# Kernel optimization log

Measured on AMD Instinct MI355X. Metric: run time of the kernel, lower is better.

Reference implementation:

```python
import jax, jax.numpy as jnp
import numpy as np

HIDDEN = 2048
NUM_HEADS = 16
HEAD_DIM = 128
ROPE_THETA = 10000.0


def setup_inputs() -> dict:
    key = jax.random.key(0)
    ks = jax.random.split(key, 5)
    s = 1.0 / np.sqrt(HIDDEN)
    return {
        "hidden_states": jax.random.normal(ks[0], (2, 2048, HIDDEN), dtype=jnp.float32),
        "wq": jax.random.normal(ks[1], (HIDDEN, HIDDEN), dtype=jnp.float32) * s,
        "wk": jax.random.normal(ks[2], (HIDDEN, HIDDEN), dtype=jnp.float32) * s,
        "wv": jax.random.normal(ks[3], (HIDDEN, HIDDEN), dtype=jnp.float32) * s,
        "wo": jax.random.normal(ks[4], (HIDDEN, HIDDEN), dtype=jnp.float32) * s,
    }


def _rope_tables(seq_len, head_dim, dtype):
    pos = jnp.arange(seq_len, dtype=jnp.float32)
    inv_freq = 1.0 / (ROPE_THETA ** (jnp.arange(0, head_dim, 2, dtype=jnp.float32) / head_dim))
    freqs = pos[:, None] * inv_freq[None, :]          # [S, D/2]
    emb = jnp.concatenate([freqs, freqs], axis=-1)    # [S, D]
    return jnp.cos(emb).astype(dtype), jnp.sin(emb).astype(dtype)


def _rotate_half(x):
    x1, x2 = jnp.split(x, 2, axis=-1)
    return jnp.concatenate([-x2, x1], axis=-1)


def reference(hidden_states, wq, wk, wv, wo):
    B, S, H = hidden_states.shape
    nh, hd = NUM_HEADS, HEAD_DIM
    # Projections (torch Linear: x @ W^T); weights stored as [out, in]
    q = (hidden_states @ wq.T).reshape(B, S, nh, hd).transpose(0, 2, 1, 3)  # [B,nh,S,hd]
    k = (hidden_states @ wk.T).reshape(B, S, nh, hd).transpose(0, 2, 1, 3)
    v = (hidden_states @ wv.T).reshape(B, S, nh, hd).transpose(0, 2, 1, 3)
    # Inline RoPE
    cos, sin = _rope_tables(S, hd, q.dtype)           # [S, hd]
    cos = cos[None, None]                             # [1,1,S,hd]
    sin = sin[None, None]
    q = q * cos + _rotate_half(q) * sin
    k = k * cos + _rotate_half(k) * sin
    # Full attention (no mask path; default pos ids)
    scores = jnp.einsum("bhqd,bhkd->bhqk", q, k) / jnp.sqrt(jnp.asarray(hd, q.dtype))
    attn = jax.nn.softmax(scores.astype(jnp.float32), axis=-1).astype(q.dtype)
    out = jnp.einsum("bhqk,bhkd->bhqd", attn, v)      # [B,nh,S,hd]
    out = out.transpose(0, 2, 1, 3).reshape(B, S, nh * hd)
    return out @ wo.T
```

## Files before the change

### kernel.cpp

```cpp
#include <hip/hip_runtime.h>
#include <hip/hip_bf16.h>
#include <math.h>

#define HIDDEN 2048
#define NH 16
#define HD 128
#define SEQ 2048
#define BATCH 2
#define NROW (BATCH*SEQ)

typedef unsigned short u16;
typedef unsigned int   u32;
typedef __bf16 bf16x8 __attribute__((ext_vector_type(8)));
typedef float  f32x4  __attribute__((ext_vector_type(4)));

__device__ __forceinline__ u16 f2bf(float f){
  u32 u = __float_as_uint(f);
  u32 r = (u + 0x7fffu + ((u >> 16) & 1u)) >> 16;
  return (u16)r;
}
__device__ __forceinline__ float bf2f(u16 h){ return __uint_as_float(((u32)h) << 16); }

typedef const void __attribute__((address_space(1)))* gas1_ptr;
typedef void __attribute__((address_space(3)))*       las3_ptr;
__device__ __forceinline__ void gload16(const void* g, void* l){
  __builtin_amdgcn_global_load_lds((gas1_ptr)g, (las3_ptr)l, 16, 0, 0);
}

__global__ void cast_kernel(const float* __restrict__ src, u16* __restrict__ dst, int n4){
  int i = blockIdx.x * blockDim.x + threadIdx.x;
  if (i >= n4) return;
  float4 v = reinterpret_cast<const float4*>(src)[i];
  ushort4 o;
  o.x = f2bf(v.x); o.y = f2bf(v.y); o.z = f2bf(v.z); o.w = f2bf(v.w);
  reinterpret_cast<ushort4*>(dst)[i] = o;
}

__global__ void rope_table_kernel(float* __restrict__ cosT, float* __restrict__ sinT){
  int i = blockIdx.x * blockDim.x + threadIdx.x;
  if (i >= SEQ * 64) return;
  int s = i >> 6, d = i & 63;
  float invf = expf(-(float)d * 0.14391156830f);
  float ang = (float)s * invf;
  float sv, cv;
  sincosf(ang, &sv, &cv);
  cosT[i] = cv; sinT[i] = sv;
}

__global__ void rope_apply_kernel(u16* __restrict__ Q, u16* __restrict__ K,
                                  const float* __restrict__ cosT, const float* __restrict__ sinT){
  int i = blockIdx.x * blockDim.x + threadIdx.x;
  if (i >= NROW * NH * 64) return;
  int d  = i & 63;
  int rh = i >> 6;
  int s  = (rh / NH) & (SEQ - 1);
  size_t base = (size_t)rh * HD;
  float c  = cosT[(s << 6) + d];
  float sn = sinT[(s << 6) + d];
  float q0 = bf2f(Q[base + d]), q1 = bf2f(Q[base + d + 64]);
  float k0 = bf2f(K[base + d]), k1 = bf2f(K[base + d + 64]);
  Q[base + d]      = f2bf(q0 * c - q1 * sn);
  Q[base + d + 64] = f2bf(q1 * c + q0 * sn);
  K[base + d]      = f2bf(k0 * c - k1 * sn);
  K[base + d + 64] = f2bf(k1 * c + k0 * sn);
}

template<int BF16OUT>
__global__ __launch_bounds__(256) void gemm_bt_kernel(
    const u16* __restrict__ A, const u16* __restrict__ B, void* __restrict__ C,
    int M, int N, int K)
{
  __shared__ __align__(16) u16 As[128 * 32];
  __shared__ __align__(16) u16 Bs[128 * 32];
  const int tid  = threadIdx.x;
  const int wid  = tid >> 6;
  const int lane = tid & 63;
  const int lrow = lane & 15, lk = lane >> 4;
  const int wr = wid >> 1, wc = wid & 1;
  const int row0 = blockIdx.x * 128, col0 = blockIdx.y * 128;

  f32x4 acc[4][4];
  #pragma unroll
  for (int m = 0; m < 4; m++)
    #pragma unroll
    for (int n = 0; n < 4; n++) acc[m][n] = (f32x4){0.f, 0.f, 0.f, 0.f};

  const int arow = tid >> 2;
  const int acol = (tid & 3) * 8;
  const u16* Ag = A + (size_t)(row0 + arow) * K + acol;
  const u16* Bg = B + (size_t)(col0 + arow) * K + acol;
  u16* AsW = As + wid * 512;
  u16* BsW = Bs + wid * 512;

  for (int k0 = 0; k0 < K; k0 += 32){
    gload16(Ag + k0,          AsW);
    gload16(Ag + 64 * K + k0, AsW + 2048);
    gload16(Bg + k0,          BsW);
    gload16(Bg + 64 * K + k0, BsW + 2048);
    __syncthreads();
    bf16x8 af[4], bfv[4];
    #pragma unroll
    for (int m = 0; m < 4; m++) af[m]  = *(const bf16x8*)&As[(wr * 64 + m * 16 + lrow) * 32 + lk * 8];
    #pragma unroll
    for (int n = 0; n < 4; n++) bfv[n] = *(const bf16x8*)&Bs[(wc * 64 + n * 16 + lrow) * 32 + lk * 8];
    #pragma unroll
    for (int m = 0; m < 4; m++)
      #pragma unroll
      for (int n = 0; n < 4; n++)
        acc[m][n] = __builtin_amdgcn_mfma_f32_16x16x32_bf16(af[m], bfv[n], acc[m][n], 0, 0, 0);
    __syncthreads();
  }

  #pragma unroll
  for (int m = 0; m < 4; m++){
    const int r = row0 + wr * 64 + m * 16 + lk * 4;
    #pragma unroll
    for (int n = 0; n < 4; n++){
      const int c = col0 + wc * 64 + n * 16 + lrow;
      #pragma unroll
      for (int j = 0; j < 4; j++){
        float v = acc[m][n][j];
        if constexpr (BF16OUT) ((u16*)C)[(size_t)(r + j) * N + c] = f2bf(v);
        else                   ((float*)C)[(size_t)(r + j) * N + c] = v;
      }
    }
  }
}

__global__ __launch_bounds__(256) void attn_kernel(
    const u16* __restrict__ Q, const u16* __restrict__ K,
    const u16* __restrict__ V, u16* __restrict__ O)
{
  __shared__ __align__(16) u16 Ks[32 * 128];
  __shared__ __align__(16) u16 Vt[128 * 32];
  __shared__ __align__(16) u16 Pl[4][16 * 32];
  const int tid = threadIdx.x, wid = tid >> 6, lane = tid & 63;
  const int lrow = lane & 15, lk = lane >> 4;
  const int b = blockIdx.z, h = blockIdx.y;
  const int q0 = blockIdx.x * 64 + wid * 16;

  bf16x8 qf[4];
  const u16* qrow = Q + ((size_t)((b * SEQ + q0 + lrow) * NH) + h) * HD;
  #pragma unroll
  for (int kc = 0; kc < 4; kc++) qf[kc] = *(const bf16x8*)(qrow + kc * 32 + lk * 8);

  f32x4 accO[8];
  #pragma unroll
  for (int i = 0; i < 8; i++) accO[i] = (f32x4){0.f, 0.f, 0.f, 0.f};
  float mrun[4] = {-1e30f, -1e30f, -1e30f, -1e30f};
  float lrun[4] = {0.f, 0.f, 0.f, 0.f};
  const float SC = 0.08838834764831845f * 1.4426950408889634f;

  const int skey = tid >> 4;
  const int spc  = tid & 15;
  const int vkey = tid & 31;
  const int vdel = (tid >> 5) * 8;
  const u16* Kbase = K + ((size_t)(b * SEQ) * NH + h) * HD;
  const u16* Vbase = V + ((size_t)(b * SEQ) * NH + h) * HD;
  u16* KsW = Ks + wid * 512;

  for (int kv = 0; kv < SEQ; kv += 32){
    __syncthreads();
    #pragma unroll
    for (int r = 0; r < 2; r++){
      int key   = r * 16 + skey;
      int cdata = spc ^ (key & 7);
      gload16(Kbase + (size_t)(kv + key) * (NH * HD) + cdata * 8, KsW + r * 2048);
    }
    #pragma unroll
    for (int r = 0; r < 2; r++){
      int dd0 = r * 64 + vdel;
      const u16* g = Vbase + (size_t)(kv + vkey) * (NH * HD) + dd0;
      uint4 vv = *(const uint4*)g;
      #pragma unroll
      for (int j = 0; j < 8; j++){
        u32 word = (j < 2) ? vv.x : (j < 4) ? vv.y : (j < 6) ? vv.z : vv.w;
        u16 val  = (u16)((j & 1) ? (word >> 16) : (word & 0xffff));
        int dd = dd0 + j;
        int c  = (vkey >> 3) ^ ((dd >> 1) & 3);
        Vt[dd * 32 + c * 8 + (vkey & 7)] = val;
      }
    }
    __syncthreads();

    f32x4 accS[2];
    accS[0] = (f32x4){0.f,0.f,0.f,0.f}; accS[1] = (f32x4){0.f,0.f,0.f,0.f};
    #pragma unroll
    for (int ns = 0; ns < 2; ns++){
      int row = ns * 16 + lrow;
      #pragma unroll
      for (int kc = 0; kc < 4; kc++){
        int pc = (kc * 4 + lk) ^ (row & 7);
        bf16x8 kf = *(const bf16x8*)&Ks[row * 128 + pc * 8];
        accS[ns] = __builtin_amdgcn_mfma_f32_16x16x32_bf16(qf[kc], kf, accS[ns], 0, 0, 0);
      }
    }

    float su[2][4], tmax[4];
    #pragma unroll
    for (int j = 0; j < 4; j++){
      su[0][j] = accS[0][j] * SC;
      su[1][j] = accS[1][j] * SC;
      tmax[j]  = fmaxf(su[0][j], su[1][j]);
    }
    #pragma unroll
    for (int j = 0; j < 4; j++){
      #pragma unroll
      for (int m = 1; m < 16; m <<= 1) tmax[j] = fmaxf(tmax[j], __shfl_xor(tmax[j], m));
    }
    float alpha[4], p[2][4];
    #pragma unroll
    for (int j = 0; j < 4; j++){
      float mnew = fmaxf(mrun[j], tmax[j]);
      alpha[j]   = exp2f(mrun[j] - mnew);
      mrun[j]    = mnew;
      p[0][j] = exp2f(su[0][j] - mnew);
      p[1][j] = exp2f(su[1][j] - mnew);
      float rowsum = p[0][j] + p[1][j];
      #pragma unroll
      for (int m = 1; m < 16; m <<= 1) rowsum += __shfl_xor(rowsum, m);
      lrun[j] = lrun[j] * alpha[j] + rowsum;
    }
    #pragma unroll
    for (int dn = 0; dn < 8; dn++)
      #pragma unroll
      for (int j = 0; j < 4; j++) accO[dn][j] *= alpha[j];

    u16* pb = &Pl[wid][0];
    #pragma unroll
    for (int ns = 0; ns < 2; ns++)
      #pragma unroll
      for (int j = 0; j < 4; j++){
        int prow = lk * 4 + j;
        int pcol = ns * 16 + lrow;
        int c = (pcol >> 3) ^ ((prow >> 1) & 3);
        pb[prow * 32 + c * 8 + (pcol & 7)] = f2bf(p[ns][j]);
      }
    int pc2 = lk ^ ((lrow >> 1) & 3);
    bf16x8 pf = *(const bf16x8*)&pb[lrow * 32 + pc2 * 8];

    #pragma unroll
    for (int dn = 0; dn < 8; dn++){
      int row = dn * 16 + lrow;
      int vc = lk ^ ((row >> 1) & 3);
      bf16x8 vf = *(const bf16x8*)&Vt[row * 32 + vc * 8];
      accO[dn] = __builtin_amdgcn_mfma_f32_16x16x32_bf16(pf, vf, accO[dn], 0, 0, 0);
    }
  }

  #pragma unroll
  for (int dn = 0; dn < 8; dn++){
    #pragma unroll
    for (int j = 0; j < 4; j++){
      int qq = q0 + lk * 4 + j;
      float v = accO[dn][j] / lrun[j];
      O[((size_t)(b * SEQ + qq) * NH + h) * HD + dn * 16 + lrow] = f2bf(v);
    }
  }
}

extern "C" void kernel_launch(void* const* d_in, const int* in_sizes, int n_in,
                              void* d_out, int out_size, void* d_ws, size_t ws_size,
                              hipStream_t stream){
  const float* hs = (const float*)d_in[0];
  const float* wq = (const float*)d_in[1];
  const float* wk = (const float*)d_in[2];
  const float* wv = (const float*)d_in[3];
  const float* wo = (const float*)d_in[4];
  float* out = (float*)d_out;

  char* ws = (char*)d_ws;
  const size_t NEL_HS = (size_t)NROW * HIDDEN;
  const size_t NEL_W  = (size_t)HIDDEN * HIDDEN;
  u16* hsb = (u16*)ws; ws += NEL_HS * 2;
  u16* wqb = (u16*)ws; ws += NEL_W * 2;
  u16* wkb = (u16*)ws; ws += NEL_W * 2;
  u16* wvb = (u16*)ws; ws += NEL_W * 2;
  u16* wob = (u16*)ws; ws += NEL_W * 2;
  u16* qb  = (u16*)ws; ws += NEL_HS * 2;
  u16* kb  = (u16*)ws; ws += NEL_HS * 2;
  u16* vb  = (u16*)ws; ws += NEL_HS * 2;
  u16* ab  = (u16*)ws; ws += NEL_HS * 2;
  float* cosT = (float*)ws; ws += (size_t)SEQ * 64 * 4;
  float* sinT = (float*)ws; ws += (size_t)SEQ * 64 * 4;

  cast_kernel<<<dim3((unsigned)(NEL_HS / 4 / 256)), dim3(256), 0, stream>>>(hs, hsb, (int)(NEL_HS / 4));
  cast_kernel<<<dim3((unsigned)(NEL_W  / 4 / 256)), dim3(256), 0, stream>>>(wq, wqb, (int)(NEL_W / 4));
  cast_kernel<<<dim3((unsigned)(NEL_W  / 4 / 256)), dim3(256), 0, stream>>>(wk, wkb, (int)(NEL_W / 4));
  cast_kernel<<<dim3((unsigned)(NEL_W  / 4 / 256)), dim3(256), 0, stream>>>(wv, wvb, (int)(NEL_W / 4));
  cast_kernel<<<dim3((unsigned)(NEL_W  / 4 / 256)), dim3(256), 0, stream>>>(wo, wob, (int)(NEL_W / 4));
  rope_table_kernel<<<dim3(SEQ * 64 / 256), dim3(256), 0, stream>>>(cosT, sinT);
  gemm_bt_kernel<1><<<dim3(NROW / 128, HIDDEN / 128), dim3(256), 0, stream>>>(hsb, wqb, qb, NROW, HIDDEN, HIDDEN);
  gemm_bt_kernel<1><<<dim3(NROW / 128, HIDDEN / 128), dim3(256), 0, stream>>>(hsb, wkb, kb, NROW, HIDDEN, HIDDEN);
  gemm_bt_kernel<1><<<dim3(NROW / 128, HIDDEN / 128), dim3(256), 0, stream>>>(hsb, wvb, vb, NROW, HIDDEN, HIDDEN);
  rope_apply_kernel<<<dim3(NROW * NH * 64 / 256), dim3(256), 0, stream>>>(qb, kb, cosT, sinT);
  attn_kernel<<<dim3(SEQ / 64, NH, BATCH), dim3(256), 0, stream>>>(qb, kb, vb, ab);
  gemm_bt_kernel<0><<<dim3(NROW / 128, HIDDEN / 128), dim3(256), 0, stream>>>(ab, wob, out, NROW, HIDDEN, HIDDEN);
}
```

Before: 623.6 us.

## Restructure flash attention with transposed score MFMA, 64-key tiles, and ds_read_tr for V

```diff
diff --git a/kernel.cpp b/kernel.cpp
--- a/kernel.cpp
+++ b/kernel.cpp
@@ -11,6 +11,7 @@
 
 typedef unsigned short u16;
 typedef unsigned int   u32;
+typedef unsigned long long u64;
 typedef __bf16 bf16x8 __attribute__((ext_vector_type(8)));
 typedef float  f32x4  __attribute__((ext_vector_type(4)));
 
@@ -131,130 +132,140 @@
     const u16* __restrict__ Q, const u16* __restrict__ K,
     const u16* __restrict__ V, u16* __restrict__ O)
 {
-  __shared__ __align__(16) u16 Ks[32 * 128];
-  __shared__ __align__(16) u16 Vt[128 * 32];
-  __shared__ __align__(16) u16 Pl[4][16 * 32];
+  __shared__ __align__(128) u16 Ks[64 * 128];
+  __shared__ __align__(128) u16 Vs[64 * 128];
   const int tid = threadIdx.x, wid = tid >> 6, lane = tid & 63;
   const int lrow = lane & 15, lk = lane >> 4;
   const int b = blockIdx.z, h = blockIdx.y;
-  const int q0 = blockIdx.x * 64 + wid * 16;
+  const int q0w = blockIdx.x * 64 + wid * 16;
+
+  const float SCL = 0.08838834764831845f * 1.4426950408889634f;
 
   bf16x8 qf[4];
-  const u16* qrow = Q + ((size_t)((b * SEQ + q0 + lrow) * NH) + h) * HD;
-  #pragma unroll
-  for (int kc = 0; kc < 4; kc++) qf[kc] = *(const bf16x8*)(qrow + kc * 32 + lk * 8);
+  {
+    const u16* qrow = Q + ((size_t)((b * SEQ + q0w + lrow) * NH) + h) * HD;
+    #pragma unroll
+    for (int kc = 0; kc < 4; kc++){
+      union { bf16x8 v; u16 s[8]; } u;
+      u.v = *(const bf16x8*)(qrow + kc * 32 + lk * 8);
+      #pragma unroll
+      for (int j = 0; j < 8; j++) u.s[j] = f2bf(bf2f(u.s[j]) * SCL);
+      qf[kc] = u.v;
+    }
+  }
 
   f32x4 accO[8];
   #pragma unroll
   for (int i = 0; i < 8; i++) accO[i] = (f32x4){0.f, 0.f, 0.f, 0.f};
-  float mrun[4] = {-1e30f, -1e30f, -1e30f, -1e30f};
-  float lrun[4] = {0.f, 0.f, 0.f, 0.f};
-  const float SC = 0.08838834764831845f * 1.4426950408889634f;
-
-  const int skey = tid >> 4;
-  const int spc  = tid & 15;
-  const int vkey = tid & 31;
-  const int vdel = (tid >> 5) * 8;
-  const u16* Kbase = K + ((size_t)(b * SEQ) * NH + h) * HD;
-  const u16* Vbase = V + ((size_t)(b * SEQ) * NH + h) * HD;
-  u16* KsW = Ks + wid * 512;
-
-  for (int kv = 0; kv < SEQ; kv += 32){
+  float mrun = -1e30f, lrun = 0.f;
+
+  const u16* Kbase = K + (size_t)(b * SEQ) * (NH * HD) + h * HD;
+  const u16* Vbase = V + (size_t)(b * SEQ) * (NH * HD) + h * HD;
+  const u32 vsbase = (u32)(size_t)(las3_ptr)&Vs[0];
+  const u32 vaddr  = vsbase + (u32)(lk * 1024 + lrow * 8);
+
+  const int ksub = lane >> 4;
+  const int kchk = lane & 15;
+  const int vsub = (lane >> 1) & 3;
+  const int vd   = (lane >> 3) * 16 + (lane & 1) * 8;
+
+  for (int kv = 0; kv < SEQ; kv += 64){
     __syncthreads();
     #pragma unroll
-    for (int r = 0; r < 2; r++){
-      int key   = r * 16 + skey;
-      int cdata = spc ^ (key & 7);
-      gload16(Kbase + (size_t)(kv + key) * (NH * HD) + cdata * 8, KsW + r * 2048);
-    }
-    #pragma unroll
-    for (int r = 0; r < 2; r++){
-      int dd0 = r * 64 + vdel;
-      const u16* g = Vbase + (size_t)(kv + vkey) * (NH * HD) + dd0;
-      uint4 vv = *(const uint4*)g;
-      #pragma unroll
-      for (int j = 0; j < 8; j++){
-        u32 word = (j < 2) ? vv.x : (j < 4) ? vv.y : (j < 6) ? vv.z : vv.w;
-        u16 val  = (u16)((j & 1) ? (word >> 16) : (word & 0xffff));
-        int dd = dd0 + j;
-        int c  = (vkey >> 3) ^ ((dd >> 1) & 3);
-        Vt[dd * 32 + c * 8 + (vkey & 7)] = val;
+    for (int r = 0; r < 4; r++){
+      int kl = wid * 16 + r * 4 + ksub;
+      int cd = kchk ^ ((r * 4 + ksub) & 7);
+      gload16(Kbase + (size_t)(kv + kl) * (NH * HD) + cd * 8,
+              (char*)Ks + (size_t)(wid * 16 + r * 4) * 256);
+    }
+    #pragma unroll
+    for (int r = 0; r < 4; r++){
+      int kl = wid * 16 + r * 4 + vsub;
+      gload16(Vbase + (size_t)(kv + kl) * (NH * HD) + vd,
+              (char*)Vs + (size_t)(wid * 4 + r) * 1024);
+    }
+    __syncthreads();
+
+    f32x4 accS[4];
+    #pragma unroll
+    for (int mb = 0; mb < 4; mb++) accS[mb] = (f32x4){0.f, 0.f, 0.f, 0.f};
+    #pragma unroll
+    for (int mb = 0; mb < 4; mb++){
+      const int key = mb * 16 + lrow;
+      #pragma unroll
+      for (int kc = 0; kc < 4; kc++){
+        int pc = (kc * 4 + lk) ^ (key & 7);
+        bf16x8 kf = *(const bf16x8*)&Ks[key * 128 + pc * 8];
+        accS[mb] = __builtin_amdgcn_mfma_f32_16x16x32_bf16(kf, qf[kc], accS[mb], 0, 0, 0);
       }
     }
-    __syncthreads();
-
-    f32x4 accS[2];
-    accS[0] = (f32x4){0.f,0.f,0.f,0.f}; accS[1] = (f32x4){0.f,0.f,0.f,0.f};
-    #pragma unroll
-    for (int ns = 0; ns < 2; ns++){
-      int row = ns * 16 + lrow;
-      #pragma unroll
-      for (int kc = 0; kc < 4; kc++){
-        int pc = (kc * 4 + lk) ^ (row & 7);
-        bf16x8 kf = *(const bf16x8*)&Ks[row * 128 + pc * 8];
-        accS[ns] = __builtin_amdgcn_mfma_f32_16x16x32_bf16(qf[kc], kf, accS[ns], 0, 0, 0);
-      }
-    }
-
-    float su[2][4], tmax[4];
+
+    float su[4][4];
+    float tmax = -1e30f;
+    #pragma unroll
+    for (int mb = 0; mb < 4; mb++)
+      #pragma unroll
+      for (int j = 0; j < 4; j++){ su[mb][j] = accS[mb][j]; tmax = fmaxf(tmax, su[mb][j]); }
+    tmax = fmaxf(tmax, __shfl_xor(tmax, 16));
+    tmax = fmaxf(tmax, __shfl_xor(tmax, 32));
+    float mnew = fmaxf(mrun, tmax);
+    if (!__all(mnew == mrun)){
+      float alpha = exp2f(mrun - mnew);
+      mrun = mnew;
+      lrun *= alpha;
+      float aj[4];
+      #pragma unroll
+      for (int j = 0; j < 4; j++) aj[j] = __shfl(alpha, lk * 4 + j, 64);
+      #pragma unroll
+      for (int dn = 0; dn < 8; dn++)
+        #pragma unroll
+        for (int j = 0; j < 4; j++) accO[dn][j] *= aj[j];
+    }
+    float rsum = 0.f;
+    float p[4][4];
+    #pragma unroll
+    for (int mb = 0; mb < 4; mb++)
+      #pragma unroll
+      for (int j = 0; j < 4; j++){ p[mb][j] = exp2f(su[mb][j] - mrun); rsum += p[mb][j]; }
+    rsum += __shfl_xor(rsum, 16);
+    rsum += __shfl_xor(rsum, 32);
+    lrun += rsum;
+
+    union { u16 s[8]; bf16x8 v; } pk0, pk1;
     #pragma unroll
     for (int j = 0; j < 4; j++){
-      su[0][j] = accS[0][j] * SC;
-      su[1][j] = accS[1][j] * SC;
-      tmax[j]  = fmaxf(su[0][j], su[1][j]);
-    }
+      pk0.s[j]     = f2bf(p[0][j]);
+      pk0.s[4 + j] = f2bf(p[1][j]);
+      pk1.s[j]     = f2bf(p[2][j]);
+      pk1.s[4 + j] = f2bf(p[3][j]);
+    }
+
+    #pragma unroll
+    for (int dn = 0; dn < 8; dn++){
+      u64 t0, t1, t2, t3;
+      asm volatile("ds_read_b64_tr_b16 %0, %1 offset:%c2" : "=v"(t0) : "v"(vaddr), "i"(dn * 128));
+      asm volatile("ds_read_b64_tr_b16 %0, %1 offset:%c2" : "=v"(t1) : "v"(vaddr), "i"(4096 + dn * 128));
+      asm volatile("ds_read_b64_tr_b16 %0, %1 offset:%c2" : "=v"(t2) : "v"(vaddr), "i"(8192 + dn * 128));
+      asm volatile("ds_read_b64_tr_b16 %0, %1 offset:%c2" : "=v"(t3) : "v"(vaddr), "i"(12288 + dn * 128));
+      asm volatile("s_waitcnt lgkmcnt(0)");
+      __builtin_amdgcn_sched_barrier(0);
+      union { u64 q[2]; bf16x8 v; } vb0, vb1;
+      vb0.q[0] = t0; vb0.q[1] = t1;
+      vb1.q[0] = t2; vb1.q[1] = t3;
+      accO[dn] = __builtin_amdgcn_mfma_f32_16x16x32_bf16(pk0.v, vb0.v, accO[dn], 0, 0, 0);
+      accO[dn] = __builtin_amdgcn_mfma_f32_16x16x32_bf16(pk1.v, vb1.v, accO[dn], 0, 0, 0);
+    }
+  }
+
+  float linv[4];
+  #pragma unroll
+  for (int j = 0; j < 4; j++) linv[j] = 1.0f / __shfl(lrun, lk * 4 + j, 64);
+  #pragma unroll
+  for (int dn = 0; dn < 8; dn++){
     #pragma unroll
     for (int j = 0; j < 4; j++){
-      #pragma unroll
-      for (int m = 1; m < 16; m <<= 1) tmax[j] = fmaxf(tmax[j], __shfl_xor(tmax[j], m));
-    }
-    float alpha[4], p[2][4];
-    #pragma unroll
-    for (int j = 0; j < 4; j++){
-      float mnew = fmaxf(mrun[j], tmax[j]);
-      alpha[j]   = exp2f(mrun[j] - mnew);
-      mrun[j]    = mnew;
-      p[0][j] = exp2f(su[0][j] - mnew);
-      p[1][j] = exp2f(su[1][j] - mnew);
-      float rowsum = p[0][j] + p[1][j];
-      #pragma unroll
-      for (int m = 1; m < 16; m <<= 1) rowsum += __shfl_xor(rowsum, m);
-      lrun[j] = lrun[j] * alpha[j] + rowsum;
-    }
-    #pragma unroll
-    for (int dn = 0; dn < 8; dn++)
-      #pragma unroll
-      for (int j = 0; j < 4; j++) accO[dn][j] *= alpha[j];
-
-    u16* pb = &Pl[wid][0];
-    #pragma unroll
-    for (int ns = 0; ns < 2; ns++)
-      #pragma unroll
-      for (int j = 0; j < 4; j++){
-        int prow = lk * 4 + j;
-        int pcol = ns * 16 + lrow;
-        int c = (pcol >> 3) ^ ((prow >> 1) & 3);
-        pb[prow * 32 + c * 8 + (pcol & 7)] = f2bf(p[ns][j]);
-      }
-    int pc2 = lk ^ ((lrow >> 1) & 3);
-    bf16x8 pf = *(const bf16x8*)&pb[lrow * 32 + pc2 * 8];
-
-    #pragma unroll
-    for (int dn = 0; dn < 8; dn++){
-      int row = dn * 16 + lrow;
-      int vc = lk ^ ((row >> 1) & 3);
-      bf16x8 vf = *(const bf16x8*)&Vt[row * 32 + vc * 8];
-      accO[dn] = __builtin_amdgcn_mfma_f32_16x16x32_bf16(pf, vf, accO[dn], 0, 0, 0);
-    }
-  }
-
-  #pragma unroll
-  for (int dn = 0; dn < 8; dn++){
-    #pragma unroll
-    for (int j = 0; j < 4; j++){
-      int qq = q0 + lk * 4 + j;
-      float v = accO[dn][j] / lrun[j];
-      O[((size_t)(b * SEQ + qq) * NH + h) * HD + dn * 16 + lrow] = f2bf(v);
+      int qq = q0w + lk * 4 + j;
+      O[((size_t)(b * SEQ + qq) * NH + h) * HD + dn * 16 + lrow] = f2bf(accO[dn][j] * linv[j]);
     }
   }
 }
```

Result: faster. 506.2 us (-18.8%).
